# Kernel tuning notes

Hardware: AMD Instinct MI355X
Metric: run time of the kernel (lower is better)

## Reference

```python
import jax, jax.numpy as jnp
import numpy as np

DIM = 64
HEADS = 1
SR = 8
EPS = 1e-5


def layer_norm(x, g, b):
    mu = jnp.mean(x, axis=-1, keepdims=True)
    var = jnp.var(x, axis=-1, keepdims=True)
    return (x - mu) * jax.lax.rsqrt(var + EPS) * g + b


def setup_inputs() -> dict:
    key = jax.random.key(0)
    ks = jax.random.split(key, 10)
    B, N, C = 8, 16384, DIM
    s = 1.0 / np.sqrt(C)
    return {
        "x": jax.random.normal(ks[0], (B, N, C), dtype=jnp.float32),
        "H": 128,
        "W": 128,
        "Wq": jax.random.normal(ks[1], (C, C), dtype=jnp.float32) * s,
        "bq": jnp.zeros((C,), jnp.float32),
        "Wkv": jax.random.normal(ks[2], (C, 2 * C), dtype=jnp.float32) * s,
        "bkv": jnp.zeros((2 * C,), jnp.float32),
        "sr_w": jax.random.normal(ks[3], (C, C, SR, SR), dtype=jnp.float32) * (1.0 / np.sqrt(C * SR * SR)),
        "sr_b": jnp.zeros((C,), jnp.float32),
        "ln_g": jnp.ones((C,), jnp.float32),
        "ln_b": jnp.zeros((C,), jnp.float32),
        "Wp": jax.random.normal(ks[4], (C, C), dtype=jnp.float32) * s,
        "bp": jnp.zeros((C,), jnp.float32),
    }


def reference(x, H, W, Wq, bq, Wkv, bkv, sr_w, sr_b, ln_g, ln_b, Wp, bp):
    B, N, C = x.shape
    h, d = HEADS, C // HEADS
    scale = d ** -0.5
    # Q at full resolution: [B, h, N, d]
    q = (x @ Wq + bq).reshape(B, N, h, d).transpose(0, 2, 1, 3)
    # Spatial reduction: conv(k=SR, stride=SR) then LayerNorm
    x2d = x.transpose(0, 2, 1).reshape(B, C, H, W)
    x2d = jax.lax.conv_general_dilated(
        x2d, sr_w, window_strides=(SR, SR), padding="VALID",
        dimension_numbers=("NCHW", "OIHW", "NCHW")) + sr_b[None, :, None, None]
    xr = x2d.reshape(B, C, -1).transpose(0, 2, 1)  # [B, Nk, C]
    xr = layer_norm(xr, ln_g, ln_b)
    # K, V on reduced sequence: [B, h, Nk, d]
    kv = (xr @ Wkv + bkv).reshape(B, -1, 2, h, d).transpose(2, 0, 3, 1, 4)
    k, v = kv[0], kv[1]
    # attn_drop(p=0) is identity; softmax over Nk
    attn = jax.nn.softmax(jnp.einsum("bhnd,bhkd->bhnk", q, k) * scale, axis=-1)
    out = jnp.einsum("bhnk,bhkd->bhnd", attn, v).transpose(0, 2, 1, 3).reshape(B, N, C)
    return out @ Wp + bp
```

## Files before the change

kernel.cpp:

```cpp
#include <hip/hip_runtime.h>
#include <hip/hip_bf16.h>
#include <math.h>


#define B 8
#define N 16384
#define C 64
#define NK 256
#define HW 128

typedef unsigned short ushort_t;
typedef unsigned int uint_t;
typedef __attribute__((ext_vector_type(8))) short short8v;
typedef __attribute__((ext_vector_type(16))) float f32x16;

static __device__ inline ushort_t f2bf(float f) {
  __hip_bfloat16 h = __float2bfloat16(f);
  return *reinterpret_cast<ushort_t*>(&h);
}
static __device__ inline uint_t cvtpk(float a, float b) {
  uint_t r;
  asm("v_cvt_pk_bf16_f32 %0, %1, %2" : "=v"(r) : "v"(a), "v"(b));
  return r;
}
static __device__ inline short8v mk8(uint_t a, uint_t b, uint_t c, uint_t d) {
  union { int4 i; short8v s; } u;
  u.i = make_int4((int)a, (int)b, (int)c, (int)d);
  return u.s;
}
static __device__ inline float sum16(const f32x16 v) {
  float a = ((v[0] + v[1]) + (v[2] + v[3])) + ((v[4] + v[5]) + (v[6] + v[7]));
  float b = ((v[8] + v[9]) + (v[10] + v[11])) + ((v[12] + v[13]) + (v[14] + v[15]));
  return a + b;
}

__global__ __launch_bounds__(256) void prep0(
    const float* __restrict__ sr_w, const float* __restrict__ Wq,
    const float* __restrict__ Wkv, const float* __restrict__ bq,
    const float* __restrict__ Wp, const float* __restrict__ bkv,
    const float* __restrict__ bp, ushort_t* __restrict__ Wf,
    ushort_t* __restrict__ W2f, float* __restrict__ u,
    float* __restrict__ bp2) {
  const int bid = blockIdx.x;
  const int t = threadIdx.x;
  const float SC = 0.125f * 1.4426950408889634f;
  if (bid < 1024) {
    int idx = bid * 256 + t;
    int o = idx >> 12;
    int r = idx & 4095;
    int c = r >> 6;
    int ki = (r >> 3) & 7;
    int kj = r & 7;
    int oh = o >> 5;
    int l = ((c >> 3) & 1) * 32 + (o & 31);
    int kk = kj * 4 + (c >> 4);
    int e = c & 7;
    Wf[(ki * 2 + oh) * 16384 + kk * 512 + l * 8 + e] = f2bf(sr_w[idx]);
  } else if (bid < 1040) {
    const int eb = bid - 1024;
#pragma unroll
    for (int q = 0; q < 2; ++q) {
      int oidx = eb * 512 + t * 2 + q;
      int mat = oidx >> 12;
      int rem = oidx & 4095;
      int d = rem >> 6;
      int c = rem & 63;
      float s = 0.f;
      if (mat == 0) {
        const float* wk = Wkv + d * 128;
        const float* wq = Wq + c * 64;
#pragma unroll 16
        for (int e = 0; e < 64; ++e) s += wk[e] * wq[e];
        s *= SC;
      } else {
        const float* wk = Wkv + d * 128 + 64;
#pragma unroll 16
        for (int e = 0; e < 64; ++e) s += wk[e] * Wp[e * 64 + c];
      }
      W2f[((mat * 2 + (c >> 5)) * 4 + (d >> 4)) * 512 +
          (((d >> 3) & 1) * 32 + (c & 31)) * 8 + (d & 7)] = f2bf(s);
    }
  } else {
    if (t < 64) {
      float s = 0.f;
      const float* wk = Wkv + t * 128;
#pragma unroll 16
      for (int e = 0; e < 64; ++e) s += wk[e] * bq[e];
      u[t] = s * SC;
    } else if (t < 128) {
      int c = t - 64;
      float s = bp[c];
#pragma unroll 16
      for (int e = 0; e < 64; ++e) s += bkv[64 + e] * Wp[e * 64 + c];
      bp2[c] = s;
    }
  }
}

__global__ __launch_bounds__(128) void conv_mfma(
    const float* __restrict__ x, const ushort_t* __restrict__ Wf,
    float* __restrict__ part) {
  const int t = threadIdx.x;
  const int bi = blockIdx.x;
  const int b = bi >> 6;
  const int pg = (bi >> 3) & 7;
  const int ki = bi & 7;
  const int oh = t >> 6;
  const int lane = t & 63;
  const int lo5 = lane & 31;
  const int hi = lane >> 5;

  const int P = pg * 32 + lo5;
  const int prow = P >> 4, pcol = P & 15;
  const float* rowbase =
      x + ((size_t)b * N + (prow * 8 + ki) * HW + pcol * 8) * C;
  const ushort_t* wbase = Wf + (ki * 2 + oh) * 16384 + lane * 8;

  f32x16 acc;
#pragma unroll
  for (int r = 0; r < 16; ++r) acc[r] = 0.f;

#pragma unroll
  for (int kk = 0; kk < 32; ++kk) {
    const int kj = kk >> 2;
    const int c0 = (kk & 3) * 16 + hi * 8;
    const float4* xp = reinterpret_cast<const float4*>(rowbase + kj * C + c0);
    float4 f0 = xp[0];
    float4 f1 = xp[1];
    short8v bfr = mk8(cvtpk(f0.x, f0.y), cvtpk(f0.z, f0.w), cvtpk(f1.x, f1.y),
                      cvtpk(f1.z, f1.w));
    short8v afr = *reinterpret_cast<const short8v*>(wbase + kk * 512);
    acc = __builtin_amdgcn_mfma_f32_32x32x16_bf16(afr, bfr, acc, 0, 0, 0);
  }

  float* dst = part + (size_t)bi * 2048 + oh * 1024 + lane * 16;
#pragma unroll
  for (int q = 0; q < 4; ++q) {
    *reinterpret_cast<float4*>(dst + 4 * q) =
        make_float4(acc[4 * q + 0], acc[4 * q + 1], acc[4 * q + 2],
                    acc[4 * q + 3]);
  }
}

__global__ __launch_bounds__(256) void ln_prep(
    const float* __restrict__ part, const float* __restrict__ sr_b,
    const float* __restrict__ ln_g, const float* __restrict__ ln_b,
    const ushort_t* __restrict__ W2f, const float* __restrict__ u,
    ushort_t* __restrict__ MTf, ushort_t* __restrict__ VpTf,
    ushort_t* __restrict__ sbf) {
  __shared__ float convs[32 * 68];
  __shared__ float ns[32 * 68];

  const int t = threadIdx.x;
  const int b = blockIdx.x >> 3;
  const int pg = blockIdx.x & 7;
  const size_t obase = (size_t)b * 16384;

  {
    const int lane = t & 63;
    const int rhalf = (t >> 6) & 1;
    const int oh = t >> 7;
    float a[8];
#pragma unroll
    for (int r = 0; r < 8; ++r) a[r] = 0.f;
#pragma unroll
    for (int ki = 0; ki < 8; ++ki) {
      const float* src = part + ((size_t)(b * 64 + pg * 8 + ki)) * 2048 +
                         oh * 1024 + lane * 16 + rhalf * 8;
      float4 u0 = *reinterpret_cast<const float4*>(src + 0);
      float4 u1 = *reinterpret_cast<const float4*>(src + 4);
      a[0] += u0.x; a[1] += u0.y; a[2] += u0.z; a[3] += u0.w;
      a[4] += u1.x; a[5] += u1.y; a[6] += u1.z; a[7] += u1.w;
    }
    const int p = lane & 31;
#pragma unroll
    for (int r = 0; r < 8; ++r) {
      int reg = rhalf * 8 + r;
      int o = oh * 32 + (reg & 3) + 8 * (reg >> 2) + 4 * (lane >> 5);
      convs[p * 68 + o] = a[r] + sr_b[o];
    }
  }
  __syncthreads();
  {
    const int lane = t & 63;
    const int w = t >> 6;
    float g = ln_g[lane], bb = ln_b[lane];
#pragma unroll
    for (int rr = 0; rr < 8; ++rr) {
      int p = w * 8 + rr;
      float v = convs[p * 68 + lane];
      float s = v, s2 = v * v;
#pragma unroll
      for (int mask = 1; mask < 64; mask <<= 1) {
        s += __shfl_xor(s, mask, 64);
        s2 += __shfl_xor(s2, mask, 64);
      }
      float mu = s * (1.f / 64.f);
      float var = s2 * (1.f / 64.f) - mu * mu;
      ns[p * 68 + lane] = (v - mu) * rsqrtf(var + 1e-5f) * g + bb;
    }
  }
  __syncthreads();
  {
    const int w = t >> 6;
    const int lane = t & 63;
    const int lo5 = lane & 31;
    const int hi = lane >> 5;
    const int mat = w >> 1;
    const int n0 = w & 1;

    f32x16 acc;
#pragma unroll
    for (int r = 0; r < 16; ++r) acc[r] = 0.f;
#pragma unroll
    for (int ks = 0; ks < 4; ++ks) {
      float4 f0 = *reinterpret_cast<const float4*>(&ns[lo5 * 68 + ks * 16 + hi * 8]);
      float4 f1 = *reinterpret_cast<const float4*>(&ns[lo5 * 68 + ks * 16 + hi * 8 + 4]);
      short8v A = mk8(cvtpk(f0.x, f0.y), cvtpk(f0.z, f0.w), cvtpk(f1.x, f1.y),
                      cvtpk(f1.z, f1.w));
      short8v Bw = *reinterpret_cast<const short8v*>(
          W2f + ((mat * 2 + n0) * 4 + ks) * 512 + lane * 8);
      acc = __builtin_amdgcn_mfma_f32_32x32x16_bf16(A, Bw, acc, 0, 0, 0);
    }
    const int c = n0 * 32 + lo5;
    if (mat == 0) {
#pragma unroll
      for (int r = 0; r < 16; ++r) {
        int jl = (r & 3) + 8 * (r >> 2) + 4 * hi;
        MTf[obase + (pg * 4 + (c >> 4)) * 512 +
            (((c >> 3) & 1) * 32 + jl) * 8 + (c & 7)] = f2bf(acc[r]);
      }
    } else {
#pragma unroll
      for (int r = 0; r < 16; ++r) {
        int jg = pg * 32 + (r & 3) + 8 * (r >> 2) + 4 * hi;
        VpTf[obase + (n0 * 16 + (jg >> 4)) * 512 +
             (((jg >> 3) & 1) * 32 + (c & 31)) * 8 + (jg & 7)] = f2bf(acc[r]);
      }
    }
    if (w == 0) {
      float s = 0.f;
      const float* ub = u + hi * 32;
#pragma unroll 8
      for (int dd = 0; dd < 32; ++dd) s += ns[lo5 * 68 + hi * 32 + dd] * ub[dd];
      s += __shfl_xor(s, 32, 64);
      if (hi == 0) sbf[b * NK + pg * 32 + lo5] = f2bf(s);
    }
  }
}

__global__ __launch_bounds__(256, 4) void attn_mfma(
    const float* __restrict__ x, const ushort_t* __restrict__ MTf,
    const ushort_t* __restrict__ VpTf, const ushort_t* __restrict__ sbf,
    const float* __restrict__ bp2, float* __restrict__ outp) {
  __shared__ ushort_t sMT[16384];
  __shared__ ushort_t sSB[256];

  const int t = threadIdx.x;
  const int b = blockIdx.x >> 7;
  const int qb = blockIdx.x & 127;
  const int wave = t >> 6;
  const int lane = t & 63;
  const int lo5 = lane & 31;
  const int hi = lane >> 5;

  const int row = qb * 128 + wave * 32 + lo5;
  const float4* xp =
      reinterpret_cast<const float4*>(x + ((size_t)b * N + row) * 64);
  float4 xf[8];
#pragma unroll
  for (int ks = 0; ks < 4; ++ks) {
    xf[2 * ks + 0] = xp[ks * 4 + hi * 2 + 0];
    xf[2 * ks + 1] = xp[ks * 4 + hi * 2 + 1];
  }

  {
    const uint4* gm = reinterpret_cast<const uint4*>(MTf + (size_t)b * 16384);
    uint4* dm = reinterpret_cast<uint4*>(sMT);
#pragma unroll
    for (int i = 0; i < 8; ++i) dm[t + i * 256] = gm[t + i * 256];
    if (t < 32)
      reinterpret_cast<uint4*>(sSB)[t] =
          reinterpret_cast<const uint4*>(sbf + b * NK)[t];
  }
  __syncthreads();

  short8v bx[4];
#pragma unroll
  for (int ks = 0; ks < 4; ++ks) {
    bx[ks] = mk8(cvtpk(xf[2 * ks].x, xf[2 * ks].y),
                 cvtpk(xf[2 * ks].z, xf[2 * ks].w),
                 cvtpk(xf[2 * ks + 1].x, xf[2 * ks + 1].y),
                 cvtpk(xf[2 * ks + 1].z, xf[2 * ks + 1].w));
  }

  const ushort_t* vt = VpTf + (size_t)b * 16384 + lane * 8;

  f32x16 o[2];
#pragma unroll
  for (int ct = 0; ct < 2; ++ct)
#pragma unroll
    for (int r = 0; r < 16; ++r) o[ct][r] = 0.f;
  float sum = 0.f;

#pragma unroll 2
  for (int kt = 0; kt < 8; ++kt) {
    f32x16 a0;
#pragma unroll
    for (int r = 0; r < 16; ++r) a0[r] = 0.f;
#pragma unroll
    for (int ks = 0; ks < 4; ++ks) {
      const short8v a =
          *reinterpret_cast<const short8v*>(&sMT[(kt * 4 + ks) * 512 + lane * 8]);
      a0 = __builtin_amdgcn_mfma_f32_32x32x16_bf16(a, bx[ks], a0, 0, 0, 0);
    }
    {
      ushort_t sv = sSB[kt * 32 + lo5];
      short8v a5 = mk8(hi ? 0u : (uint_t)sv, 0u, 0u, 0u);
      short8v b5 = mk8(hi ? 0u : 0x3F80u, 0u, 0u, 0u);
      a0 = __builtin_amdgcn_mfma_f32_32x32x16_bf16(a5, b5, a0, 0, 0, 0);
    }
#pragma unroll
    for (int r = 0; r < 16; ++r) a0[r] = exp2f(a0[r]);
    sum += sum16(a0);
#pragma unroll
    for (int h = 0; h < 2; ++h) {
      const int m0 = 2 * h;
      uint_t Aw = cvtpk(a0[4 * m0 + 0], a0[4 * m0 + 1]);
      uint_t Bw = cvtpk(a0[4 * m0 + 2], a0[4 * m0 + 3]);
      uint_t Cw = cvtpk(a0[4 * m0 + 4], a0[4 * m0 + 5]);
      uint_t Dw = cvtpk(a0[4 * m0 + 6], a0[4 * m0 + 7]);
      asm volatile("v_permlane32_swap_b32 %0, %1" : "+v"(Aw), "+v"(Cw));
      asm volatile("v_permlane32_swap_b32 %0, %1" : "+v"(Bw), "+v"(Dw));
      const short8v pb = mk8(Aw, Bw, Cw, Dw);
#pragma unroll
      for (int ct = 0; ct < 2; ++ct) {
        const short8v va = *reinterpret_cast<const short8v*>(
            vt + (ct * 16 + kt * 2 + h) * 512);
        o[ct] = __builtin_amdgcn_mfma_f32_32x32x16_bf16(va, pb, o[ct], 0, 0, 0);
      }
    }
  }

  sum += __shfl_xor(sum, 32, 64);
  const float linv = 1.f / sum;

  float* orow = outp + ((size_t)b * N + row) * 64;
#pragma unroll
  for (int ct = 0; ct < 2; ++ct) {
#pragma unroll
    for (int mm = 0; mm < 4; ++mm) {
      int c0 = ct * 32 + mm * 8 + hi * 4;
      float4 bpv = *reinterpret_cast<const float4*>(bp2 + c0);
      float4 r;
      r.x = o[ct][4 * mm + 0] * linv + bpv.x;
      r.y = o[ct][4 * mm + 1] * linv + bpv.y;
      r.z = o[ct][4 * mm + 2] * linv + bpv.z;
      r.w = o[ct][4 * mm + 3] * linv + bpv.w;
      *reinterpret_cast<float4*>(orow + c0) = r;
    }
  }
}

extern "C" void kernel_launch(void* const* d_in, const int* in_sizes, int n_in,
                              void* d_out, int out_size, void* d_ws,
                              size_t ws_size, hipStream_t stream) {
  const float* x    = (const float*)d_in[0];
  const float* Wq   = (const float*)d_in[3];
  const float* bq   = (const float*)d_in[4];
  const float* Wkv  = (const float*)d_in[5];
  const float* bkv  = (const float*)d_in[6];
  const float* sr_w = (const float*)d_in[7];
  const float* sr_b = (const float*)d_in[8];
  const float* ln_g = (const float*)d_in[9];
  const float* ln_b = (const float*)d_in[10];
  const float* Wp   = (const float*)d_in[11];
  const float* bp   = (const float*)d_in[12];
  float* outp = (float*)d_out;

  char* ws = (char*)d_ws;
  ushort_t* Wf   = (ushort_t*)(ws);
  ushort_t* W2f  = (ushort_t*)(ws + (512 << 10));
  float*    u    = (float*)(ws + (528 << 10));
  float*    bp2  = (float*)(ws + (528 << 10) + 256);
  float*    part = (float*)(ws + (1024 << 10));
  ushort_t* MTf  = (ushort_t*)(ws + (5120 << 10));
  ushort_t* VpTf = (ushort_t*)(ws + (5376 << 10));
  ushort_t* sbf  = (ushort_t*)(ws + (5632 << 10));

  prep0<<<1041, 256, 0, stream>>>(sr_w, Wq, Wkv, bq, Wp, bkv, bp, Wf, W2f, u, bp2);
  conv_mfma<<<512, 128, 0, stream>>>(x, Wf, part);
  ln_prep<<<64, 256, 0, stream>>>(part, sr_b, ln_g, ln_b, W2f, u, MTf, VpTf, sbf);
  attn_mfma<<<1024, 256, 0, stream>>>(x, MTf, VpTf, sbf, bp2, outp);
}
```

Before: 59.98 us.

## Split conv reduction across twice the blocks, interleave batch in block index, prefetch V

The conv kernel now splits its 32-step reduction into two halves across twice as many blocks, and ln_prep sums sixteen partials instead of eight. The part buffer doubles, so the downstream workspace offsets move. All three kernels remap the block index so batch varies fastest, which spreads each batch's blocks across the GPU. The attention kernel fully unrolls its key-tile loop and prefetches the next V fragments into registers ahead of the exp/MFMA work. This trades more partial-sum traffic and register pressure for more conv parallelism and better latency hiding.

```diff
diff --git a/kernel.cpp b/kernel.cpp
--- a/kernel.cpp
+++ b/kernel.cpp
@@ -102,9 +102,10 @@
     float* __restrict__ part) {
   const int t = threadIdx.x;
   const int bi = blockIdx.x;
-  const int b = bi >> 6;
+  const int b = bi & 7;
   const int pg = (bi >> 3) & 7;
-  const int ki = bi & 7;
+  const int ki = (bi >> 6) & 7;
+  const int half = bi >> 9;
   const int oh = t >> 6;
   const int lane = t & 63;
   const int lo5 = lane & 31;
@@ -121,7 +122,8 @@
   for (int r = 0; r < 16; ++r) acc[r] = 0.f;
 
 #pragma unroll
-  for (int kk = 0; kk < 32; ++kk) {
+  for (int kkl = 0; kkl < 16; ++kkl) {
+    const int kk = half * 16 + kkl;
     const int kj = kk >> 2;
     const int c0 = (kk & 3) * 16 + hi * 8;
     const float4* xp = reinterpret_cast<const float4*>(rowbase + kj * C + c0);
@@ -152,8 +154,8 @@
   __shared__ float ns[32 * 68];
 
   const int t = threadIdx.x;
-  const int b = blockIdx.x >> 3;
-  const int pg = blockIdx.x & 7;
+  const int b = blockIdx.x & 7;
+  const int pg = blockIdx.x >> 3;
   const size_t obase = (size_t)b * 16384;
 
   {
@@ -164,9 +166,10 @@
 #pragma unroll
     for (int r = 0; r < 8; ++r) a[r] = 0.f;
 #pragma unroll
-    for (int ki = 0; ki < 8; ++ki) {
-      const float* src = part + ((size_t)(b * 64 + pg * 8 + ki)) * 2048 +
-                         oh * 1024 + lane * 16 + rhalf * 8;
+    for (int k2 = 0; k2 < 16; ++k2) {
+      int bi = b + (pg << 3) + ((k2 & 7) << 6) + ((k2 >> 3) << 9);
+      const float* src = part + (size_t)bi * 2048 + oh * 1024 + lane * 16 +
+                         rhalf * 8;
       float4 u0 = *reinterpret_cast<const float4*>(src + 0);
       float4 u1 = *reinterpret_cast<const float4*>(src + 4);
       a[0] += u0.x; a[1] += u0.y; a[2] += u0.z; a[3] += u0.w;
@@ -257,8 +260,8 @@
   __shared__ ushort_t sSB[256];
 
   const int t = threadIdx.x;
-  const int b = blockIdx.x >> 7;
-  const int qb = blockIdx.x & 127;
+  const int b = blockIdx.x & 7;
+  const int qb = blockIdx.x >> 3;
   const int wave = t >> 6;
   const int lane = t & 63;
   const int lo5 = lane & 31;
@@ -303,7 +306,12 @@
     for (int r = 0; r < 16; ++r) o[ct][r] = 0.f;
   float sum = 0.f;
 
-#pragma unroll 2
+  short8v va0 = *reinterpret_cast<const short8v*>(vt + (0 * 16 + 0) * 512);
+  short8v va1 = *reinterpret_cast<const short8v*>(vt + (1 * 16 + 0) * 512);
+  short8v va2 = *reinterpret_cast<const short8v*>(vt + (0 * 16 + 1) * 512);
+  short8v va3 = *reinterpret_cast<const short8v*>(vt + (1 * 16 + 1) * 512);
+
+#pragma unroll
   for (int kt = 0; kt < 8; ++kt) {
     f32x16 a0;
 #pragma unroll
@@ -319,6 +327,14 @@
       short8v a5 = mk8(hi ? 0u : (uint_t)sv, 0u, 0u, 0u);
       short8v b5 = mk8(hi ? 0u : 0x3F80u, 0u, 0u, 0u);
       a0 = __builtin_amdgcn_mfma_f32_32x32x16_bf16(a5, b5, a0, 0, 0, 0);
+    }
+    short8v vn0, vn1, vn2, vn3;
+    if (kt < 7) {
+      const int ksn = (kt + 1) * 2;
+      vn0 = *reinterpret_cast<const short8v*>(vt + (0 * 16 + ksn + 0) * 512);
+      vn1 = *reinterpret_cast<const short8v*>(vt + (1 * 16 + ksn + 0) * 512);
+      vn2 = *reinterpret_cast<const short8v*>(vt + (0 * 16 + ksn + 1) * 512);
+      vn3 = *reinterpret_cast<const short8v*>(vt + (1 * 16 + ksn + 1) * 512);
     }
 #pragma unroll
     for (int r = 0; r < 16; ++r) a0[r] = exp2f(a0[r]);
@@ -333,13 +349,15 @@
       asm volatile("v_permlane32_swap_b32 %0, %1" : "+v"(Aw), "+v"(Cw));
       asm volatile("v_permlane32_swap_b32 %0, %1" : "+v"(Bw), "+v"(Dw));
       const short8v pb = mk8(Aw, Bw, Cw, Dw);
-#pragma unroll
-      for (int ct = 0; ct < 2; ++ct) {
-        const short8v va = *reinterpret_cast<const short8v*>(
-            vt + (ct * 16 + kt * 2 + h) * 512);
-        o[ct] = __builtin_amdgcn_mfma_f32_32x32x16_bf16(va, pb, o[ct], 0, 0, 0);
+      if (h == 0) {
+        o[0] = __builtin_amdgcn_mfma_f32_32x32x16_bf16(va0, pb, o[0], 0, 0, 0);
+        o[1] = __builtin_amdgcn_mfma_f32_32x32x16_bf16(va1, pb, o[1], 0, 0, 0);
+      } else {
+        o[0] = __builtin_amdgcn_mfma_f32_32x32x16_bf16(va2, pb, o[0], 0, 0, 0);
+        o[1] = __builtin_amdgcn_mfma_f32_32x32x16_bf16(va3, pb, o[1], 0, 0, 0);
       }
     }
+    if (kt < 7) { va0 = vn0; va1 = vn1; va2 = vn2; va3 = vn3; }
   }
 
   sum += __shfl_xor(sum, 32, 64);
@@ -384,12 +402,12 @@
   float*    u    = (float*)(ws + (528 << 10));
   float*    bp2  = (float*)(ws + (528 << 10) + 256);
   float*    part = (float*)(ws + (1024 << 10));
-  ushort_t* MTf  = (ushort_t*)(ws + (5120 << 10));
-  ushort_t* VpTf = (ushort_t*)(ws + (5376 << 10));
-  ushort_t* sbf  = (ushort_t*)(ws + (5632 << 10));
+  ushort_t* MTf  = (ushort_t*)(ws + (9216 << 10));
+  ushort_t* VpTf = (ushort_t*)(ws + (9472 << 10));
+  ushort_t* sbf  = (ushort_t*)(ws + (9728 << 10));
 
   prep0<<<1041, 256, 0, stream>>>(sr_w, Wq, Wkv, bq, Wp, bkv, bp, Wf, W2f, u, bp2);
-  conv_mfma<<<512, 128, 0, stream>>>(x, Wf, part);
+  conv_mfma<<<1024, 128, 0, stream>>>(x, Wf, part);
   ln_prep<<<64, 256, 0, stream>>>(part, sr_b, ln_g, ln_b, W2f, u, MTf, VpTf, sbf);
   attn_mfma<<<1024, 256, 0, stream>>>(x, MTf, VpTf, sbf, bp2, outp);
 }
```

Result: slower. 96.83 us (+61.4%).
